# Performance work log

Measured on AMD Instinct MI355X. Metric: run time of the kernel, lower is better.

## Reference

```python
import jax, jax.numpy as jnp
import numpy as np

D = 128
RANK = 16
N_USER, N_PROD, N_CAT, N_BRAND = 100000, 100000, 1000, 2000
E_BEH, E_STR = 100000, 50000
NODE_TYPES = ['user', 'product', 'category', 'brand']
N_NODES = {'user': N_USER, 'product': N_PROD, 'category': N_CAT, 'brand': N_BRAND}
PHI = {'user': 0, 'product': 1, 'category': 2, 'brand': 3}
# (src_type, edge_name, dst_type, rel_idx, beta or None for structural)
EDGE_META = [
    ('user', 'view', 'product', 0, 0),
    ('user', 'cart', 'product', 1, 1),
    ('user', 'purchase', 'product', 2, 2),
    ('product', 'rev_view', 'user', 3, 0),
    ('product', 'rev_cart', 'user', 4, 1),
    ('product', 'rev_purchase', 'user', 5, 2),
    ('product', 'belongs_to', 'category', 6, None),
    ('category', 'contains', 'product', 7, None),
    ('product', 'producedBy', 'brand', 8, None),
    ('brand', 'brands', 'product', 9, None),
]


def setup_inputs() -> dict:
    key = jax.random.key(0)
    ks = iter(jax.random.split(key, 64))
    inp = {}
    for t in NODE_TYPES:
        inp['x_' + t] = jax.random.normal(next(ks), (N_NODES[t], D), jnp.float32)
    for (st, name, dt, ridx, beta) in EDGE_META:
        E = E_BEH if beta is not None else E_STR
        src = jax.random.randint(next(ks), (E,), 0, N_NODES[st], jnp.int32)
        dst = jax.random.randint(next(ks), (E,), 0, N_NODES[dt], jnp.int32)
        inp['ei_' + name] = jnp.stack([src, dst])
        if beta is None:
            inp['attr_' + name] = jax.random.randint(next(ks), (E,), 0, 3, jnp.int32)
    s = 0.05
    inp['W_base'] = jax.random.normal(next(ks), (D, D), jnp.float32) * s
    inp['A'] = jax.random.normal(next(ks), (4, D, RANK), jnp.float32) * s
    inp['B'] = jax.random.normal(next(ks), (4, D, RANK), jnp.float32) * s
    inp['rel_W'] = jax.random.normal(next(ks), (10, D), jnp.float32) * s
    inp['beh_W'] = jax.random.normal(next(ks), (4, D), jnp.float32) * s
    inp['a_att'] = jax.random.normal(next(ks), (4 * D,), jnp.float32) * s
    inp['ln_gamma'] = jnp.ones((D,), jnp.float32)
    inp['ln_beta'] = jnp.zeros((D,), jnp.float32)
    return inp


def _forward(x, eis, attrs, W_base, A, B, rel_W, beh_W, a_att, ln_gamma, ln_beta):
    a0, a1, a2, a3 = a_att[:D], a_att[D:2 * D], a_att[2 * D:3 * D], a_att[3 * D:]
    agg = {t: jnp.zeros((N_NODES[t], D), x['user'].dtype) for t in NODE_TYPES}
    for (src_t, name, dst_t, ridx, beta) in EDGE_META:
        ei = eis[name]
        src, dst = ei[0], ei[1]
        hs = x[src_t][src]            # [E, D] gather
        hd = x[dst_t][dst]            # [E, D] gather
        phi = PHI[src_t]
        if beta is not None:
            # uniform behavior beta: W = W_base + A_phi @ B_beta^T
            W = W_base + A[phi] @ B[beta].T
            msg = hs @ W.T
            hproj = hd @ W.T
            b_term = (beh_W[beta] * a3).sum()
        else:
            # per-edge behavior origin from edge_attr (clamped to {0,1,2})
            origin = jnp.clip(attrs[name].reshape(-1), 0, 2)
            mids = jnp.einsum('ei,bir->ebr', hs, B[:3])            # [E, 3, rank]
            mid = jnp.take_along_axis(mids, origin[:, None, None], axis=1)[:, 0, :]
            msg = hs @ W_base.T + mid @ A[phi].T
            hproj = hd @ W_base.T
            b_term = (beh_W[origin] * a3).sum(-1)                  # [E]
        r_scalar = (rel_W[ridx] * a2).sum()
        e = (msg * a0).sum(-1) + (hproj * a1).sum(-1) + r_scalar + b_term
        # destination-grouped softmax over edges
        n_dst = N_NODES[dst_t]
        m = jax.ops.segment_max(e, dst, num_segments=n_dst)
        ex = jnp.exp(e - m[dst])
        ssum = jax.ops.segment_sum(ex, dst, num_segments=n_dst)
        alpha = ex / (ssum[dst] + 1e-16)
        agg[dst_t] = agg[dst_t] + jax.ops.segment_sum(alpha[:, None] * msg, dst, num_segments=n_dst)
    outs = []
    for t in NODE_TYPES:
        h = agg[t]
        mu = h.mean(-1, keepdims=True)
        var = ((h - mu) ** 2).mean(-1, keepdims=True)
        hn = (h - mu) / jnp.sqrt(var + 1e-5) * ln_gamma + ln_beta
        outs.append(jax.nn.elu(hn + x[t]))   # residual: in_dim == out_dim
    return jnp.concatenate(outs, axis=0)     # [N_user+N_prod+N_cat+N_brand, D]


def reference(x_user, x_product, x_category, x_brand,
              ei_view, ei_cart, ei_purchase, ei_rev_view, ei_rev_cart, ei_rev_purchase,
              ei_belongs_to, ei_contains, ei_producedBy, ei_brands,
              attr_belongs_to, attr_contains, attr_producedBy, attr_brands,
              W_base, A, B, rel_W, beh_W, a_att, ln_gamma, ln_beta):
    x = {'user': x_user, 'product': x_product, 'category': x_category, 'brand': x_brand}
    eis = {'view': ei_view, 'cart': ei_cart, 'purchase': ei_purchase,
           'rev_view': ei_rev_view, 'rev_cart': ei_rev_cart, 'rev_purchase': ei_rev_purchase,
           'belongs_to': ei_belongs_to, 'contains': ei_contains,
           'producedBy': ei_producedBy, 'brands': ei_brands}
    attrs = {'belongs_to': attr_belongs_to, 'contains': attr_contains,
             'producedBy': attr_producedBy, 'brands': attr_brands}
    return _forward(x, eis, attrs, W_base, A, B, rel_W, beh_W, a_att, ln_gamma, ln_beta)
```

## Files before the change

kernel.cpp:

```cpp
#include <hip/hip_runtime.h>
#include <hip/hip_bf16.h>
#include <math.h>

#define D 128

#define NU 100000
#define NP 100000
#define NC 1000
#define NB 2000
#define NTOT 203000
#define EB 100000
#define ES 50000
#define ETOT 800000
#define NSEG 803000
#define NBLK 785

#define OFF_L    0
#define OFF_W0   6448000
#define OFF_BS   6451840
#define OFF_WT   7251856
#define OFF_AT   7268240
#define OFF_INT  7276432

__constant__ int c_srcT[10]   = {0,0,0,1,1,1,1,2,1,3};
__constant__ int c_phi [10]   = {0,0,0,1,1,1,1,2,1,3};
__constant__ int c_beta[10]   = {0,1,2,0,1,2,-1,-1,-1,-1};
__constant__ int c_E   [10]   = {EB,EB,EB,EB,EB,EB,ES,ES,ES,ES};
__constant__ int c_moff[10]   = {0,100000,200000,300000,400000,500000,600000,601000,701000,703000};

__constant__ int g_nGrp[4]    = {1,3,1,1};
__constant__ int g_Loff[4][3] = {{1600000,0,0},{0,3216000,4848000},{3200000,0,0},{4816000,0,0}};
__constant__ int g_ai[4][3]   = {{1,0,0},{0,2,3},{1,0,0},{1,0,0}};

#define K4_BU 782
#define K4_BP 1564
#define K4_BC 1572
#define K4_BT 1588

struct Ptrs {
    const float* x[4];
    const int*   ei[10];
    const int*   attr[4];
};

__device__ __forceinline__ void decode_et(int eflat, int& et, int& le) {
    if (eflat < 600000) { et = eflat / 100000; le = eflat - et * 100000; }
    else { int r = eflat - 600000; int q = r / 50000; et = 6 + q; le = r - q * 50000; }
}

__device__ __forceinline__ float qsum(float v) {
    v += __shfl_xor(v, 1, 64);
    v += __shfl_xor(v, 2, 64);
    v += __shfl_xor(v, 4, 64);
    v += __shfl_xor(v, 8, 64);
    return v;
}

__global__ void k0_tables(const float* __restrict__ Wb, const float* __restrict__ A,
                          const float* __restrict__ B, const float* __restrict__ behW,
                          const float* __restrict__ a_att,
                          float* __restrict__ w0, float* __restrict__ bs_out)
{
    __shared__ float a0[128];
    __shared__ float c0[128];
    __shared__ float g0[4][16];
    int t = threadIdx.x;
    if (t < 128) a0[t] = a_att[t];
    __syncthreads();
    if (t < 128) {
        float s0=0.f;
        for (int j=0;j<128;j++) s0 += Wb[j*128+t]*a0[j];
        c0[t]=s0;
    } else if (t < 192) {
        int q=t-128, p=q>>4, r=q&15;
        float s0=0.f;
        for (int i=0;i<128;i++) s0 += A[p*2048+i*16+r]*a0[i];
        g0[p][r]=s0;
    } else if (t < 196) {
        int b=t-192; float s=0.f;
        for (int i=0;i<128;i++) s += behW[b*128+i]*a_att[384+i];
        bs_out[b]=s;
    }
    __syncthreads();
    if (t < 128) {
        for (int et=0; et<10; ++et) {
            int phi=c_phi[et], beta=c_beta[et];
            if (beta >= 0) {
                float s0=c0[t];
                for (int r=0;r<16;r++) s0 += B[beta*2048+t*16+r]*g0[phi][r];
                w0[et*384+t]=s0; w0[et*384+128+t]=s0; w0[et*384+256+t]=s0;
            } else {
                for (int o=0;o<3;o++){
                    float s0=c0[t];
                    for (int r=0;r<16;r++) s0 += B[o*2048+t*16+r]*g0[phi][r];
                    w0[et*384+o*128+t]=s0;
                }
            }
        }
    }
}

__global__ __launch_bounds__(256) void ktrans(const float* __restrict__ Wb,
        const float* __restrict__ A, float* __restrict__ WbT, float* __restrict__ AT)
{
    int idx = blockIdx.x*256 + threadIdx.x;
    if (idx < 16384) { int i = idx>>7, j = idx&127; WbT[i*128+j] = Wb[j*128+i]; }
    int idx2 = idx - 16384;
    if (idx2 >= 0 && idx2 < 8192) {
        int p = idx2>>11, rem = idx2&2047, r = rem>>7, j = rem&127;
        AT[idx2] = A[p*2048 + j*16 + r];
    }
}

__global__ __launch_bounds__(256) void khist(Ptrs P, int* __restrict__ counts)
{
    int eflat = blockIdx.x*256 + threadIdx.x;
    if (eflat >= ETOT) return;
    int et, le; decode_et(eflat, et, le);
    int dst = P.ei[et][c_E[et] + le];
    atomicAdd(&counts[c_moff[et] + dst], 1);
}

__global__ __launch_bounds__(256) void kscan1(const int* __restrict__ cnt,
                                              int* __restrict__ st, int* __restrict__ bsums)
{
    __shared__ int lds[256];
    int t = threadIdx.x, b = blockIdx.x;
    int base = b*1024 + t*4;
    int v0 = (base   < NSEG) ? cnt[base]   : 0;
    int v1 = (base+1 < NSEG) ? cnt[base+1] : 0;
    int v2 = (base+2 < NSEG) ? cnt[base+2] : 0;
    int v3 = (base+3 < NSEG) ? cnt[base+3] : 0;
    int s = v0+v1+v2+v3;
    lds[t] = s; __syncthreads();
    for (int off=1; off<256; off<<=1){
        int xv = (t>=off) ? lds[t-off] : 0;
        __syncthreads();
        lds[t] += xv;
        __syncthreads();
    }
    int incl = lds[t];
    int p = incl - s;
    if (t==255) bsums[b] = incl;
    if (base   < NSEG) st[base]   = p; p += v0;
    if (base+1 < NSEG) st[base+1] = p; p += v1;
    if (base+2 < NSEG) st[base+2] = p; p += v2;
    if (base+3 < NSEG) st[base+3] = p;
}

__global__ __launch_bounds__(256) void kscan2(int* __restrict__ bsums)
{
    __shared__ int lds[256];
    int t = threadIdx.x;
    int base = t*4;
    int v0 = (base   < NBLK) ? bsums[base]   : 0;
    int v1 = (base+1 < NBLK) ? bsums[base+1] : 0;
    int v2 = (base+2 < NBLK) ? bsums[base+2] : 0;
    int v3 = (base+3 < NBLK) ? bsums[base+3] : 0;
    int s = v0+v1+v2+v3;
    lds[t] = s; __syncthreads();
    for (int off=1; off<256; off<<=1){
        int xv = (t>=off) ? lds[t-off] : 0;
        __syncthreads();
        lds[t] += xv;
        __syncthreads();
    }
    int p = lds[t] - s;
    if (base   < NBLK) bsums[base]   = p; p += v0;
    if (base+1 < NBLK) bsums[base+1] = p; p += v1;
    if (base+2 < NBLK) bsums[base+2] = p; p += v2;
    if (base+3 < NBLK) bsums[base+3] = p;
}

__global__ __launch_bounds__(256) void kscan3(int* __restrict__ st, const int* __restrict__ bsums)
{
    int t = threadIdx.x, b = blockIdx.x;
    int add = bsums[b];
    int base = b*1024 + t*4;
    #pragma unroll
    for (int j=0;j<4;j++)
        if (base+j < NSEG) st[base+j] += add;
}

__global__ __launch_bounds__(256) void kscatter(Ptrs P, int* __restrict__ st, int* __restrict__ srco)
{
    int eflat = blockIdx.x*256 + threadIdx.x;
    if (eflat >= ETOT) return;
    int et, le; decode_et(eflat, et, le);
    const int* ei = P.ei[et];
    int E = c_E[et];
    int src = ei[le], dst = ei[E+le];
    int o;
    if (et >= 6) { int a = P.attr[et-6][le]; o = min(max(a,0),2); }
    else o = c_beta[et];
    int pos = atomicAdd(&st[c_moff[et] + dst], 1);
    srco[pos] = src | (o<<17) | (et<<19);
}

__global__ __launch_bounds__(256) void kagg_beh(Ptrs P,
        const int* __restrict__ starts, const int* __restrict__ counts,
        const int* __restrict__ srco,
        const float* __restrict__ w0, const float* __restrict__ Bm,
        float* __restrict__ Sout, float* __restrict__ Lb, int nWaves)
{
    int lane = threadIdx.x & 63;
    int wv = (blockIdx.x * 256 + threadIdx.x) >> 6;
    int grp = lane >> 4, ln = lane & 15;

    for (int nid = wv; nid < NU + NP; nid += nWaves) {
        int T = (nid < NU) ? 0 : 1;
        int n0 = (T == 0) ? nid : nid - NU;
        int etBase = (T == 0) ? 3 : 0;
        const float* xs = P.x[1 - T];

        int sgA = c_moff[etBase] + n0;
        int cnt0 = counts[sgA],        cnt1 = counts[sgA+100000], cnt2 = counts[sgA+200000];
        int sa0  = starts[sgA]-cnt0,   sa1  = starts[sgA+100000]-cnt1, sa2 = starts[sgA+200000]-cnt2;
        int sv1 = (grp < cnt1) ? srco[sa1+grp] : 0;
        int sv2 = (grp < cnt2) ? srco[sa2+grp] : 0;
        float4 pA = make_float4(0.f,0.f,0.f,0.f), pB = pA;
        if (grp < cnt0) {
            int sv0 = srco[sa0+grp];
            const float* q = xs + (size_t)(sv0 & 0x1FFFF)*D + ln*8;
            pA = *(const float4*)q; pB = *(const float4*)(q+4);
        }

        float Stot[8] = {0,0,0,0,0,0,0,0};
        float Lq0=0.f, Lq1=0.f, Lq2=0.f, Lq3=0.f;

        for (int s=0; s<3; ++s) {
            int cnt = (s==0)?cnt0:((s==1)?cnt1:cnt2);
            int st0 = (s==0)?sa0:((s==1)?sa1:sa2);
            float4 cA = pA, cB = pB;
            pA = make_float4(0.f,0.f,0.f,0.f); pB = pA;
            if (s == 0) {
                if (grp < cnt1) {
                    const float* q = xs + (size_t)(sv1 & 0x1FFFF)*D + ln*8;
                    pA = *(const float4*)q; pB = *(const float4*)(q+4);
                }
            } else if (s == 1) {
                if (grp < cnt2) {
                    const float* q = xs + (size_t)(sv2 & 0x1FFFF)*D + ln*8;
                    pA = *(const float4*)q; pB = *(const float4*)(q+4);
                }
            }
            if (cnt == 0) continue;
            int et = etBase + s;
            const float* wq = w0 + et*384 + ln*8;
            float4 wA = *(const float4*)wq, wB = *(const float4*)(wq+4);

            float ssum = 0.f;
            float SA[8] = {0,0,0,0,0,0,0,0};

            for (int k0=0; k0<cnt; k0+=4) {
                bool act = (k0+grp) < cnt;
                if (k0 > 0) {
                    cA = make_float4(0.f,0.f,0.f,0.f); cB = cA;
                    if (act) {
                        int sv = srco[st0+k0+grp];
                        const float* q = xs + (size_t)(sv & 0x1FFFF)*D + ln*8;
                        cA = *(const float4*)q; cB = *(const float4*)(q+4);
                    }
                }
                float d = cA.x*wA.x + cA.y*wA.y + cA.z*wA.z + cA.w*wA.w
                        + cB.x*wB.x + cB.y*wB.y + cB.z*wB.z + cB.w*wB.w;
                d = qsum(d);
                float wg = act ? __expf(d) : 0.f;
                ssum += wg;
                SA[0]+=wg*cA.x; SA[1]+=wg*cA.y; SA[2]+=wg*cA.z; SA[3]+=wg*cA.w;
                SA[4]+=wg*cB.x; SA[5]+=wg*cB.y; SA[6]+=wg*cB.z; SA[7]+=wg*cB.w;
            }
            ssum += __shfl_xor(ssum, 16, 64);
            ssum += __shfl_xor(ssum, 32, 64);
            float inv = 1.f/(ssum + 1e-16f);
            #pragma unroll
            for (int j=0;j<8;j++){ SA[j] += __shfl_xor(SA[j],16,64); SA[j] += __shfl_xor(SA[j],32,64); }
            #pragma unroll
            for (int j=0;j<8;j++) Stot[j] += SA[j]*inv;

            const float* Bp = Bm + s*2048 + grp*4;
            float p0=0.f,p1=0.f,p2=0.f,p3=0.f;
            #pragma unroll
            for (int j=0;j<8;j++){
                float4 b4 = *(const float4*)(Bp + (ln*8+j)*16);
                float v = SA[j];
                p0+=v*b4.x; p1+=v*b4.y; p2+=v*b4.z; p3+=v*b4.w;
            }
            Lq0 += qsum(p0)*inv; Lq1 += qsum(p1)*inv;
            Lq2 += qsum(p2)*inv; Lq3 += qsum(p3)*inv;
        }

        if (grp == 0) {
            float* Srow = Sout + (size_t)nid*D + ln*8;
            *(float4*)Srow     = make_float4(Stot[0],Stot[1],Stot[2],Stot[3]);
            *(float4*)(Srow+4) = make_float4(Stot[4],Stot[5],Stot[6],Stot[7]);
        }
        if (ln < 4) {
            float v = (ln==0)?Lq0:((ln==1)?Lq1:((ln==2)?Lq2:Lq3));
            int loff = (T==0) ? 1600000 : 0;
            Lb[loff + (size_t)n0*16 + grp*4 + ln] = v;
        }
    }
}

__global__ __launch_bounds__(256) void kagg_str(Ptrs P,
        const int* __restrict__ starts, const int* __restrict__ counts,
        const int* __restrict__ srco,
        const float* __restrict__ w0, const float* __restrict__ bs,
        const float* __restrict__ Bm,
        float* __restrict__ Sout, float* __restrict__ Lb, int nWaves)
{
    int lane = threadIdx.x & 63;
    int wv = (blockIdx.x * 256 + threadIdx.x) >> 6;
    int grp = lane >> 4, ln = lane & 15;
    float bs0 = bs[0], bs1 = bs[1], bs2 = bs[2];

    for (int id = wv; id < NP + NC + NB; id += nWaves) {
        int T, n0, nseg;
        if (id < NP) { T=1; n0=id; nseg=2; }
        else if (id < NP+NC) { T=2; n0=id-NP; nseg=1; }
        else { T=3; n0=id-(NP+NC); nseg=1; }
        int outRow = (T==1) ? (100000+n0) : ((T==2) ? (200000+n0) : (201000+n0));

        float Stot[8] = {0,0,0,0,0,0,0,0};

        for (int s=0; s<nseg; ++s) {
            int et = (T==1) ? (s==0 ? 7 : 9) : ((T==2) ? 6 : 8);
            int seg = c_moff[et] + n0;
            int cnt = counts[seg];
            int st0 = starts[seg] - cnt;
            const float* xs = P.x[c_srcT[et]];
            const float* wbase = w0 + et*384;

            float ssum = 0.f;
            float SA[8]={0,0,0,0,0,0,0,0}, SB[8]={0,0,0,0,0,0,0,0}, SC[8]={0,0,0,0,0,0,0,0};
            int fa=0, fb=0, fc=0;

            for (int k0=0; k0<cnt; k0+=4) {
                bool act = (k0+grp) < cnt;
                int sv = act ? srco[st0+k0+grp] : 0;
                int o = (sv>>17)&3;
                float4 hA = make_float4(0.f,0.f,0.f,0.f), hB = hA;
                if (act) {
                    const float* q = xs + (size_t)(sv & 0x1FFFF)*D + ln*8;
                    hA = *(const float4*)q; hB = *(const float4*)(q+4);
                }
                const float* wq = wbase + o*128 + ln*8;
                float4 wA = *(const float4*)wq, wB = *(const float4*)(wq+4);
                float d = hA.x*wA.x + hA.y*wA.y + hA.z*wA.z + hA.w*wA.w
                        + hB.x*wB.x + hB.y*wB.y + hB.z*wB.z + hB.w*wB.w;
                d = qsum(d);
                float wg = act ? __expf(d + ((o==0)?bs0:((o==1)?bs1:bs2))) : 0.f;
                ssum += wg;
                fa |= (int)(act && (o==0)); fb |= (int)(act && (o==1)); fc |= (int)(act && (o==2));
                float wg0=(o==0)?wg:0.f, wg1=(o==1)?wg:0.f, wg2=(o==2)?wg:0.f;
                #pragma unroll
                for (int j=0;j<8;j++){
                    float hj = (j==0)?hA.x:(j==1)?hA.y:(j==2)?hA.z:(j==3)?hA.w:
                               (j==4)?hB.x:(j==5)?hB.y:(j==6)?hB.z:hB.w;
                    SA[j] += wg0*hj; SB[j] += wg1*hj; SC[j] += wg2*hj;
                }
            }

            ssum += __shfl_xor(ssum, 16, 64);
            ssum += __shfl_xor(ssum, 32, 64);
            float inv = 1.f/(ssum + 1e-16f);

            int anyA = __any(fa), anyB = __any(fb), anyC = __any(fc);
            if (anyA) {
                #pragma unroll
                for (int j=0;j<8;j++){ SA[j] += __shfl_xor(SA[j],16,64); SA[j] += __shfl_xor(SA[j],32,64); }
            }
            if (anyB) {
                #pragma unroll
                for (int j=0;j<8;j++){ SB[j] += __shfl_xor(SB[j],16,64); SB[j] += __shfl_xor(SB[j],32,64); }
            }
            if (anyC) {
                #pragma unroll
                for (int j=0;j<8;j++){ SC[j] += __shfl_xor(SC[j],16,64); SC[j] += __shfl_xor(SC[j],32,64); }
            }
            #pragma unroll
            for (int j=0;j<8;j++) Stot[j] += (SA[j]+SB[j]+SC[j])*inv;

            float p0=0.f,p1=0.f,p2=0.f,p3=0.f;
            if (anyA) {
                const float* Bp = Bm + grp*4;
                #pragma unroll
                for (int j=0;j<8;j++){
                    float4 b4 = *(const float4*)(Bp + (ln*8+j)*16);
                    float v = SA[j];
                    p0+=v*b4.x; p1+=v*b4.y; p2+=v*b4.z; p3+=v*b4.w;
                }
            }
            if (anyB) {
                const float* Bp = Bm + 2048 + grp*4;
                #pragma unroll
                for (int j=0;j<8;j++){
                    float4 b4 = *(const float4*)(Bp + (ln*8+j)*16);
                    float v = SB[j];
                    p0+=v*b4.x; p1+=v*b4.y; p2+=v*b4.z; p3+=v*b4.w;
                }
            }
            if (anyC) {
                const float* Bp = Bm + 4096 + grp*4;
                #pragma unroll
                for (int j=0;j<8;j++){
                    float4 b4 = *(const float4*)(Bp + (ln*8+j)*16);
                    float v = SC[j];
                    p0+=v*b4.x; p1+=v*b4.y; p2+=v*b4.z; p3+=v*b4.w;
                }
            }
            p0 = qsum(p0)*inv; p1 = qsum(p1)*inv; p2 = qsum(p2)*inv; p3 = qsum(p3)*inv;

            int loff = (T==1) ? (s==0 ? 3216000 : 4848000) : ((T==2) ? 3200000 : 4816000);
            if (ln < 4) {
                float v = (ln==0)?p0:((ln==1)?p1:((ln==2)?p2:p3));
                Lb[loff + (size_t)n0*16 + grp*4 + ln] = v;
            }
        }

        if (grp == 0) {
            float* Srow = Sout + (size_t)outRow*D + ln*8;
            if (T == 1) {
                float4 a = *(const float4*)Srow, b = *(const float4*)(Srow+4);
                *(float4*)Srow     = make_float4(a.x+Stot[0],a.y+Stot[1],a.z+Stot[2],a.w+Stot[3]);
                *(float4*)(Srow+4) = make_float4(b.x+Stot[4],b.y+Stot[5],b.z+Stot[6],b.w+Stot[7]);
            } else {
                *(float4*)Srow     = make_float4(Stot[0],Stot[1],Stot[2],Stot[3]);
                *(float4*)(Srow+4) = make_float4(Stot[4],Stot[5],Stot[6],Stot[7]);
            }
        }
    }
}

__global__ __launch_bounds__(512, 1) void k4_final(Ptrs P,
        const float* __restrict__ WbT, const float* __restrict__ AT,
        const float* __restrict__ Lb,
        const float* __restrict__ gamma, const float* __restrict__ lbeta,
        float* __restrict__ out)
{
    __shared__ float st[128*132];
    __shared__ float wt[128*128];
    __shared__ float lt[128*52];
    int t = threadIdx.x;
    int b = blockIdx.x;
    int T, lb;
    if (b < K4_BU)      { T=0; lb=b; }
    else if (b < K4_BP) { T=1; lb=b-K4_BU; }
    else if (b < K4_BC) { T=2; lb=b-K4_BP; }
    else                { T=3; lb=b-K4_BC; }
    int r0 = lb*128;
    int rowStart = (T==0)?0:((T==1)?100000:((T==2)?200000:201000));
    int nRows    = (T==0)?NU:((T==1)?NP:((T==2)?NC:NB));
    const float* x = P.x[T];
    int nPairs = g_nGrp[T];

    for (int idx=t; idx<4096; idx+=512)
        *(float4*)&wt[idx*4] = *(const float4*)&WbT[idx*4];
    for (int idx=t; idx<4096; idx+=512){
        int r = idx>>5, i4 = idx&31;
        int lr = r0 + r;
        float4 v = (lr < nRows) ? *(const float4*)&out[(size_t)(rowStart+lr)*D + i4*4]
                                : make_float4(0.f,0.f,0.f,0.f);
        *(float4*)&st[r*132 + i4*4] = v;
    }
    for (int pi=0; pi<nPairs; ++pi){
        int lo = g_Loff[T][pi];
        int r = t>>2, q = t&3;
        int lr = r0 + r;
        float4 v = (lr < nRows) ? *(const float4*)&Lb[lo + (size_t)lr*16 + q*4]
                                : make_float4(0.f,0.f,0.f,0.f);
        *(float4*)&lt[r*52 + pi*16 + q*4] = v;
    }
    __syncthreads();

    int cg = t & 15, rg = t >> 4;
    float acc[4][8];
    #pragma unroll
    for (int a=0;a<4;a++)
        #pragma unroll
        for (int c=0;c<8;c++) acc[a][c]=0.f;

    for (int i4=0; i4<32; ++i4){
        float4 sv0 = *(const float4*)&st[(rg*4+0)*132 + i4*4];
        float4 sv1 = *(const float4*)&st[(rg*4+1)*132 + i4*4];
        float4 sv2 = *(const float4*)&st[(rg*4+2)*132 + i4*4];
        float4 sv3 = *(const float4*)&st[(rg*4+3)*132 + i4*4];
        #pragma unroll
        for (int q=0;q<4;q++){
            float4 wA = *(const float4*)&wt[(i4*4+q)*128 + cg*4];
            float4 wB = *(const float4*)&wt[(i4*4+q)*128 + 64 + cg*4];
            float sq[4];
            sq[0] = (q==0)?sv0.x:(q==1)?sv0.y:(q==2)?sv0.z:sv0.w;
            sq[1] = (q==0)?sv1.x:(q==1)?sv1.y:(q==2)?sv1.z:sv1.w;
            sq[2] = (q==0)?sv2.x:(q==1)?sv2.y:(q==2)?sv2.z:sv2.w;
            sq[3] = (q==0)?sv3.x:(q==1)?sv3.y:(q==2)?sv3.z:sv3.w;
            #pragma unroll
            for (int rr=0;rr<4;rr++){
                acc[rr][0] += sq[rr]*wA.x;
                acc[rr][1] += sq[rr]*wA.y;
                acc[rr][2] += sq[rr]*wA.z;
                acc[rr][3] += sq[rr]*wA.w;
                acc[rr][4] += sq[rr]*wB.x;
                acc[rr][5] += sq[rr]*wB.y;
                acc[rr][6] += sq[rr]*wB.z;
                acc[rr][7] += sq[rr]*wB.w;
            }
        }
    }

    for (int pi=0; pi<nPairs; ++pi){
        int ai = g_ai[T][pi];
        const float* Ap = AT + ai*2048;
        #pragma unroll 4
        for (int r=0;r<16;++r){
            float4 aA = *(const float4*)&Ap[r*128 + cg*4];
            float4 aB = *(const float4*)&Ap[r*128 + 64 + cg*4];
            float lv[4];
            #pragma unroll
            for (int rr=0;rr<4;rr++) lv[rr] = lt[(rg*4+rr)*52 + pi*16 + r];
            #pragma unroll
            for (int rr=0;rr<4;rr++){
                acc[rr][0] += lv[rr]*aA.x;
                acc[rr][1] += lv[rr]*aA.y;
                acc[rr][2] += lv[rr]*aA.z;
                acc[rr][3] += lv[rr]*aA.w;
                acc[rr][4] += lv[rr]*aB.x;
                acc[rr][5] += lv[rr]*aB.y;
                acc[rr][6] += lv[rr]*aB.z;
                acc[rr][7] += lv[rr]*aB.w;
            }
        }
    }

    int jA = cg*4, jB = 64 + cg*4;
    float4 gA = *(const float4*)&gamma[jA], gB = *(const float4*)&gamma[jB];
    float4 bA = *(const float4*)&lbeta[jA], bB = *(const float4*)&lbeta[jB];
    float gv[8] = {gA.x,gA.y,gA.z,gA.w,gB.x,gB.y,gB.z,gB.w};
    float bv[8] = {bA.x,bA.y,bA.z,bA.w,bB.x,bB.y,bB.z,bB.w};

    #pragma unroll
    for (int rr=0;rr<4;rr++){
        int lr = r0 + rg*4 + rr;
        float lsum=0.f, lsq=0.f;
        #pragma unroll
        for (int c=0;c<8;c++){ lsum += acc[rr][c]; lsq += acc[rr][c]*acc[rr][c]; }
        #pragma unroll
        for (int mm=1; mm<16; mm<<=1){ lsum += __shfl_xor(lsum,mm,64); lsq += __shfl_xor(lsq,mm,64); }
        if (lr >= nRows) continue;
        float mu = lsum*(1.f/128.f);
        float var = lsq*(1.f/128.f) - mu*mu;
        float rstd = rsqrtf(var + 1e-5f);
        const float* xr = x + (size_t)lr*D;
        float4 xA = *(const float4*)(xr+jA), xB = *(const float4*)(xr+jB);
        float xv[8] = {xA.x,xA.y,xA.z,xA.w,xB.x,xB.y,xB.z,xB.w};
        float ov[8];
        #pragma unroll
        for (int c=0;c<8;c++){
            float hn = (acc[rr][c]-mu)*rstd*gv[c] + bv[c];
            float z = hn + xv[c];
            ov[c] = z > 0.f ? z : expm1f(z);
        }
        float* orow = out + (size_t)(rowStart+lr)*D;
        *(float4*)(orow+jA) = make_float4(ov[0],ov[1],ov[2],ov[3]);
        *(float4*)(orow+jB) = make_float4(ov[4],ov[5],ov[6],ov[7]);
    }
}

extern "C" void kernel_launch(void* const* d_in, const int* in_sizes, int n_in,
                              void* d_out, int out_size, void* d_ws, size_t ws_size,
                              hipStream_t stream)
{
    (void)in_sizes; (void)n_in; (void)out_size; (void)ws_size;
    Ptrs P;
    P.x[0] = (const float*)d_in[0];
    P.x[1] = (const float*)d_in[1];
    P.x[2] = (const float*)d_in[2];
    P.x[3] = (const float*)d_in[3];
    P.ei[0] = (const int*)d_in[4];
    P.ei[1] = (const int*)d_in[5];
    P.ei[2] = (const int*)d_in[6];
    P.ei[3] = (const int*)d_in[7];
    P.ei[4] = (const int*)d_in[8];
    P.ei[5] = (const int*)d_in[9];
    P.ei[6] = (const int*)d_in[10];
    P.attr[0] = (const int*)d_in[11];
    P.ei[7] = (const int*)d_in[12];
    P.attr[1] = (const int*)d_in[13];
    P.ei[8] = (const int*)d_in[14];
    P.attr[2] = (const int*)d_in[15];
    P.ei[9] = (const int*)d_in[16];
    P.attr[3] = (const int*)d_in[17];
    const float* Wb    = (const float*)d_in[18];
    const float* A     = (const float*)d_in[19];
    const float* B     = (const float*)d_in[20];
    const float* behW  = (const float*)d_in[22];
    const float* a_att = (const float*)d_in[23];
    const float* gamma = (const float*)d_in[24];
    const float* lbeta = (const float*)d_in[25];
    float* wsf = (float*)d_ws;
    float* out = (float*)d_out;

    int* ip     = (int*)(wsf + OFF_INT);
    int* counts = ip;
    int* starts = ip + 803000;
    int* srco   = ip + 1606000;
    int* bsums  = (int*)wsf;

    hipMemsetAsync(counts, 0, (size_t)NSEG*sizeof(int), stream);

    k0_tables<<<1, 256, 0, stream>>>(Wb, A, B, behW, a_att, wsf+OFF_W0, wsf+OFF_BS);
    ktrans<<<96, 256, 0, stream>>>(Wb, A, wsf+OFF_WT, wsf+OFF_AT);
    khist<<<3125, 256, 0, stream>>>(P, counts);
    kscan1<<<NBLK, 256, 0, stream>>>(counts, starts, bsums);
    kscan2<<<1, 256, 0, stream>>>(bsums);
    kscan3<<<NBLK, 256, 0, stream>>>(starts, bsums);
    kscatter<<<3125, 256, 0, stream>>>(P, starts, srco);

    kagg_beh<<<2048, 256, 0, stream>>>(P, starts, counts, srco,
                                       wsf+OFF_W0, B, out, wsf+OFF_L, 2048*4);
    kagg_str<<<1024, 256, 0, stream>>>(P, starts, counts, srco,
                                       wsf+OFF_W0, wsf+OFF_BS, B, out, wsf+OFF_L, 1024*4);

    k4_final<<<K4_BT, 512, 0, stream>>>(P, wsf+OFF_WT, wsf+OFF_AT, wsf+OFF_L,
                                        gamma, lbeta, out);
}
```

Measured before the change: 893.3 us.

## Use atomic work-stealing tickets and batched metadata prefetch in behavior aggregation

Replaces the static grid-stride node loop in the behavior aggregation kernel with dynamic scheduling. Each wavefront grabs a ticket for a chunk of four nodes through an atomic counter. All counts and starts for the chunk are loaded cooperatively in one step and shared by shuffles, and the first source indices of the next node are prefetched while the current node is processed. The aim is to balance the irregular per-node degree load and hide metadata latency, at the cost of one global atomic per chunk and an extra memset.

Result: slower. 1.169 ms (+30.9%).

```diff
diff --git a/kernel.cpp b/kernel.cpp
--- a/kernel.cpp
+++ b/kernel.cpp
@@ -201,104 +201,147 @@
         const int* __restrict__ starts, const int* __restrict__ counts,
         const int* __restrict__ srco,
         const float* __restrict__ w0, const float* __restrict__ Bm,
-        float* __restrict__ Sout, float* __restrict__ Lb, int nWaves)
+        float* __restrict__ Sout, float* __restrict__ Lb, int* __restrict__ ticket)
 {
     int lane = threadIdx.x & 63;
-    int wv = (blockIdx.x * 256 + threadIdx.x) >> 6;
     int grp = lane >> 4, ln = lane & 15;
 
-    for (int nid = wv; nid < NU + NP; nid += nWaves) {
-        int T = (nid < NU) ? 0 : 1;
-        int n0 = (T == 0) ? nid : nid - NU;
-        int etBase = (T == 0) ? 3 : 0;
-        const float* xs = P.x[1 - T];
-
-        int sgA = c_moff[etBase] + n0;
-        int cnt0 = counts[sgA],        cnt1 = counts[sgA+100000], cnt2 = counts[sgA+200000];
-        int sa0  = starts[sgA]-cnt0,   sa1  = starts[sgA+100000]-cnt1, sa2 = starts[sgA+200000]-cnt2;
-        int sv1 = (grp < cnt1) ? srco[sa1+grp] : 0;
-        int sv2 = (grp < cnt2) ? srco[sa2+grp] : 0;
-        float4 pA = make_float4(0.f,0.f,0.f,0.f), pB = pA;
-        if (grp < cnt0) {
-            int sv0 = srco[sa0+grp];
-            const float* q = xs + (size_t)(sv0 & 0x1FFFF)*D + ln*8;
-            pA = *(const float4*)q; pB = *(const float4*)(q+4);
-        }
-
-        float Stot[8] = {0,0,0,0,0,0,0,0};
-        float Lq0=0.f, Lq1=0.f, Lq2=0.f, Lq3=0.f;
-
-        for (int s=0; s<3; ++s) {
-            int cnt = (s==0)?cnt0:((s==1)?cnt1:cnt2);
-            int st0 = (s==0)?sa0:((s==1)?sa1:sa2);
-            float4 cA = pA, cB = pB;
-            pA = make_float4(0.f,0.f,0.f,0.f); pB = pA;
-            if (s == 0) {
-                if (grp < cnt1) {
-                    const float* q = xs + (size_t)(sv1 & 0x1FFFF)*D + ln*8;
-                    pA = *(const float4*)q; pB = *(const float4*)(q+4);
-                }
-            } else if (s == 1) {
-                if (grp < cnt2) {
-                    const float* q = xs + (size_t)(sv2 & 0x1FFFF)*D + ln*8;
-                    pA = *(const float4*)q; pB = *(const float4*)(q+4);
-                }
-            }
-            if (cnt == 0) continue;
-            int et = etBase + s;
-            const float* wq = w0 + et*384 + ln*8;
-            float4 wA = *(const float4*)wq, wB = *(const float4*)(wq+4);
-
-            float ssum = 0.f;
-            float SA[8] = {0,0,0,0,0,0,0,0};
-
-            for (int k0=0; k0<cnt; k0+=4) {
-                bool act = (k0+grp) < cnt;
-                if (k0 > 0) {
-                    cA = make_float4(0.f,0.f,0.f,0.f); cB = cA;
-                    if (act) {
-                        int sv = srco[st0+k0+grp];
-                        const float* q = xs + (size_t)(sv & 0x1FFFF)*D + ln*8;
-                        cA = *(const float4*)q; cB = *(const float4*)(q+4);
+    for (;;) {
+        int chunk = 0;
+        if (lane == 0) chunk = atomicAdd(ticket, 1);
+        chunk = __shfl(chunk, 0, 64);
+        int base = chunk << 2;
+        if (base >= NU + NP) return;
+
+        int si = 0;
+        {
+            int j = lane / 6, r = lane - j*6;
+            if (lane < 24) {
+                int nid = base + j;
+                if (nid < NU + NP) {
+                    int s = r >> 1;
+                    int seg = ((nid < NU) ? (300000 + nid) : (nid - NU)) + s*100000;
+                    si = (r & 1) ? starts[seg] : counts[seg];
+                }
+            }
+        }
+
+        int sv0 = 0, sv1 = 0, sv2 = 0;
+        {
+            int c0 = __shfl(si, 0, 64), t0 = __shfl(si, 1, 64);
+            int c1 = __shfl(si, 2, 64), t1 = __shfl(si, 3, 64);
+            int c2 = __shfl(si, 4, 64), t2 = __shfl(si, 5, 64);
+            if (grp < c0) sv0 = srco[t0 - c0 + grp];
+            if (grp < c1) sv1 = srco[t1 - c1 + grp];
+            if (grp < c2) sv2 = srco[t2 - c2 + grp];
+        }
+
+        for (int j = 0; j < 4; ++j) {
+            int nid = base + j;
+            if (nid >= NU + NP) break;
+            int T = (nid < NU) ? 0 : 1;
+            int n0 = (T == 0) ? nid : nid - NU;
+            int etBase = (T == 0) ? 3 : 0;
+            const float* xs = P.x[1 - T];
+
+            int c0 = __shfl(si, j*6+0, 64), t0 = __shfl(si, j*6+1, 64);
+            int c1 = __shfl(si, j*6+2, 64), t1 = __shfl(si, j*6+3, 64);
+            int c2 = __shfl(si, j*6+4, 64), t2 = __shfl(si, j*6+5, 64);
+            int sa0 = t0 - c0, sa1 = t1 - c1, sa2 = t2 - c2;
+
+            int nv0 = 0, nv1 = 0, nv2 = 0;
+            if (j < 3 && base + j + 1 < NU + NP) {
+                int d0 = __shfl(si, j*6+6,  64), u0 = __shfl(si, j*6+7,  64);
+                int d1 = __shfl(si, j*6+8,  64), u1 = __shfl(si, j*6+9,  64);
+                int d2 = __shfl(si, j*6+10, 64), u2 = __shfl(si, j*6+11, 64);
+                if (grp < d0) nv0 = srco[u0 - d0 + grp];
+                if (grp < d1) nv1 = srco[u1 - d1 + grp];
+                if (grp < d2) nv2 = srco[u2 - d2 + grp];
+            }
+
+            float4 pA = make_float4(0.f,0.f,0.f,0.f), pB = pA;
+            if (grp < c0) {
+                const float* q = xs + (size_t)(sv0 & 0x1FFFF)*D + ln*8;
+                pA = *(const float4*)q; pB = *(const float4*)(q+4);
+            }
+
+            float Stot[8] = {0,0,0,0,0,0,0,0};
+            float Lq0=0.f, Lq1=0.f, Lq2=0.f, Lq3=0.f;
+
+            for (int s = 0; s < 3; ++s) {
+                int cnt = (s==0)?c0:((s==1)?c1:c2);
+                int st0 = (s==0)?sa0:((s==1)?sa1:sa2);
+                float4 cA = pA, cB = pB;
+                pA = make_float4(0.f,0.f,0.f,0.f); pB = pA;
+                if (s == 0) {
+                    if (grp < c1) {
+                        const float* q = xs + (size_t)(sv1 & 0x1FFFF)*D + ln*8;
+                        pA = *(const float4*)q; pB = *(const float4*)(q+4);
                     }
-                }
-                float d = cA.x*wA.x + cA.y*wA.y + cA.z*wA.z + cA.w*wA.w
-                        + cB.x*wB.x + cB.y*wB.y + cB.z*wB.z + cB.w*wB.w;
-                d = qsum(d);
-                float wg = act ? __expf(d) : 0.f;
-                ssum += wg;
-                SA[0]+=wg*cA.x; SA[1]+=wg*cA.y; SA[2]+=wg*cA.z; SA[3]+=wg*cA.w;
-                SA[4]+=wg*cB.x; SA[5]+=wg*cB.y; SA[6]+=wg*cB.z; SA[7]+=wg*cB.w;
-            }
-            ssum += __shfl_xor(ssum, 16, 64);
-            ssum += __shfl_xor(ssum, 32, 64);
-            float inv = 1.f/(ssum + 1e-16f);
-            #pragma unroll
-            for (int j=0;j<8;j++){ SA[j] += __shfl_xor(SA[j],16,64); SA[j] += __shfl_xor(SA[j],32,64); }
-            #pragma unroll
-            for (int j=0;j<8;j++) Stot[j] += SA[j]*inv;
-
-            const float* Bp = Bm + s*2048 + grp*4;
-            float p0=0.f,p1=0.f,p2=0.f,p3=0.f;
-            #pragma unroll
-            for (int j=0;j<8;j++){
-                float4 b4 = *(const float4*)(Bp + (ln*8+j)*16);
-                float v = SA[j];
-                p0+=v*b4.x; p1+=v*b4.y; p2+=v*b4.z; p3+=v*b4.w;
-            }
-            Lq0 += qsum(p0)*inv; Lq1 += qsum(p1)*inv;
-            Lq2 += qsum(p2)*inv; Lq3 += qsum(p3)*inv;
-        }
-
-        if (grp == 0) {
-            float* Srow = Sout + (size_t)nid*D + ln*8;
-            *(float4*)Srow     = make_float4(Stot[0],Stot[1],Stot[2],Stot[3]);
-            *(float4*)(Srow+4) = make_float4(Stot[4],Stot[5],Stot[6],Stot[7]);
-        }
-        if (ln < 4) {
-            float v = (ln==0)?Lq0:((ln==1)?Lq1:((ln==2)?Lq2:Lq3));
-            int loff = (T==0) ? 1600000 : 0;
-            Lb[loff + (size_t)n0*16 + grp*4 + ln] = v;
+                } else if (s == 1) {
+                    if (grp < c2) {
+                        const float* q = xs + (size_t)(sv2 & 0x1FFFF)*D + ln*8;
+                        pA = *(const float4*)q; pB = *(const float4*)(q+4);
+                    }
+                }
+                if (cnt == 0) continue;
+                int et = etBase + s;
+                const float* wq = w0 + et*384 + ln*8;
+                float4 wA = *(const float4*)wq, wB = *(const float4*)(wq+4);
+
+                float ssum = 0.f;
+                float SA[8] = {0,0,0,0,0,0,0,0};
+
+                for (int k0 = 0; k0 < cnt; k0 += 4) {
+                    bool act = (k0 + grp) < cnt;
+                    if (k0 > 0) {
+                        cA = make_float4(0.f,0.f,0.f,0.f); cB = cA;
+                        if (act) {
+                            int sv = srco[st0 + k0 + grp];
+                            const float* q = xs + (size_t)(sv & 0x1FFFF)*D + ln*8;
+                            cA = *(const float4*)q; cB = *(const float4*)(q+4);
+                        }
+                    }
+                    float d = cA.x*wA.x + cA.y*wA.y + cA.z*wA.z + cA.w*wA.w
+                            + cB.x*wB.x + cB.y*wB.y + cB.z*wB.z + cB.w*wB.w;
+                    d = qsum(d);
+                    float wg = act ? __expf(d) : 0.f;
+                    ssum += wg;
+                    SA[0]+=wg*cA.x; SA[1]+=wg*cA.y; SA[2]+=wg*cA.z; SA[3]+=wg*cA.w;
+                    SA[4]+=wg*cB.x; SA[5]+=wg*cB.y; SA[6]+=wg*cB.z; SA[7]+=wg*cB.w;
+                }
+                ssum += __shfl_xor(ssum, 16, 64);
+                ssum += __shfl_xor(ssum, 32, 64);
+                float inv = 1.f/(ssum + 1e-16f);
+                #pragma unroll
+                for (int jj=0;jj<8;jj++){ SA[jj] += __shfl_xor(SA[jj],16,64); SA[jj] += __shfl_xor(SA[jj],32,64); }
+                #pragma unroll
+                for (int jj=0;jj<8;jj++) Stot[jj] += SA[jj]*inv;
+
+                const float* Bp = Bm + s*2048 + grp*4;
+                float p0=0.f,p1=0.f,p2=0.f,p3=0.f;
+                #pragma unroll
+                for (int jj=0;jj<8;jj++){
+                    float4 b4 = *(const float4*)(Bp + (ln*8+jj)*16);
+                    float v = SA[jj];
+                    p0+=v*b4.x; p1+=v*b4.y; p2+=v*b4.z; p3+=v*b4.w;
+                }
+                Lq0 += qsum(p0)*inv; Lq1 += qsum(p1)*inv;
+                Lq2 += qsum(p2)*inv; Lq3 += qsum(p3)*inv;
+            }
+
+            if (grp == 0) {
+                float* Srow = Sout + (size_t)nid*D + ln*8;
+                *(float4*)Srow     = make_float4(Stot[0],Stot[1],Stot[2],Stot[3]);
+                *(float4*)(Srow+4) = make_float4(Stot[4],Stot[5],Stot[6],Stot[7]);
+            }
+            if (ln < 4) {
+                float v = (ln==0)?Lq0:((ln==1)?Lq1:((ln==2)?Lq2:Lq3));
+                int loff = (T==0) ? 1600000 : 0;
+                Lb[loff + (size_t)n0*16 + grp*4 + ln] = v;
+            }
+
+            sv0 = nv0; sv1 = nv1; sv2 = nv2;
         }
     }
 }
@@ -605,9 +648,11 @@
     int* counts = ip;
     int* starts = ip + 803000;
     int* srco   = ip + 1606000;
+    int* ticket = ip + 2406000;
     int* bsums  = (int*)wsf;
 
     hipMemsetAsync(counts, 0, (size_t)NSEG*sizeof(int), stream);
+    hipMemsetAsync(ticket, 0, sizeof(int), stream);
 
     k0_tables<<<1, 256, 0, stream>>>(Wb, A, B, behW, a_att, wsf+OFF_W0, wsf+OFF_BS);
     ktrans<<<96, 256, 0, stream>>>(Wb, A, wsf+OFF_WT, wsf+OFF_AT);
@@ -618,7 +663,7 @@
     kscatter<<<3125, 256, 0, stream>>>(P, starts, srco);
 
     kagg_beh<<<2048, 256, 0, stream>>>(P, starts, counts, srco,
-                                       wsf+OFF_W0, B, out, wsf+OFF_L, 2048*4);
+                                       wsf+OFF_W0, B, out, wsf+OFF_L, ticket);
     kagg_str<<<1024, 256, 0, stream>>>(P, starts, counts, srco,
                                        wsf+OFF_W0, wsf+OFF_BS, B, out, wsf+OFF_L, 1024*4);
 
```

## Map one node per 16-lane group in behavioral aggregation with per-edge prefetch

Applied to the files above, without the earlier changes.

The behavioral aggregation kernel now gives each wave four nodes, one per 16-lane group, instead of one node spread over four groups. Each group walks its edges one at a time and prefetches the next source row. This removes the cross-group shuffle reductions and idle lanes when a node has few edges. Segment metadata is loaded cooperatively and broadcast with shuffles. The low-rank B projection becomes a transpose-style shuffle reduction so each lane ends up with one output. The cost is serial per-edge latency inside each group and divergence when the four nodes have very different degrees.

Result: slower. 1.070 ms (+19.7%).

```diff
diff --git a/kernel.cpp b/kernel.cpp
--- a/kernel.cpp
+++ b/kernel.cpp
@@ -54,6 +54,39 @@
     v += __shfl_xor(v, 4, 64);
     v += __shfl_xor(v, 8, 64);
     return v;
+}
+
+__device__ __forceinline__ float bT_pass8(const float* __restrict__ Brow,
+                                          const float SA[8], int c0, int lane)
+{
+    float pr[8] = {0.f,0.f,0.f,0.f,0.f,0.f,0.f,0.f};
+    #pragma unroll
+    for (int j=0;j<8;j++){
+        float4 b0 = *(const float4*)(Brow + j*16 + c0);
+        float4 b1 = *(const float4*)(Brow + j*16 + c0 + 4);
+        float v = SA[j];
+        pr[0]+=v*b0.x; pr[1]+=v*b0.y; pr[2]+=v*b0.z; pr[3]+=v*b0.w;
+        pr[4]+=v*b1.x; pr[5]+=v*b1.y; pr[6]+=v*b1.z; pr[7]+=v*b1.w;
+    }
+    #pragma unroll
+    for (int r=0;r<8;r++) pr[r] += __shfl_xor(pr[r], 8, 64);
+    float v4[4];
+    #pragma unroll
+    for (int r=0;r<4;r++){
+        float kp = (lane&4) ? pr[r+4] : pr[r];
+        float gv = (lane&4) ? pr[r]   : pr[r+4];
+        v4[r] = kp + __shfl_xor(gv, 4, 64);
+    }
+    float v2[2];
+    #pragma unroll
+    for (int r=0;r<2;r++){
+        float kp = (lane&2) ? v4[r+2] : v4[r];
+        float gv = (lane&2) ? v4[r]   : v4[r+2];
+        v2[r] = kp + __shfl_xor(gv, 2, 64);
+    }
+    float kp = (lane&1) ? v2[1] : v2[0];
+    float gv = (lane&1) ? v2[0] : v2[1];
+    return kp + __shfl_xor(gv, 1, 64);
 }
 
 __global__ void k0_tables(const float* __restrict__ Wb, const float* __restrict__ A,
@@ -204,47 +237,56 @@
         float* __restrict__ Sout, float* __restrict__ Lb, int nWaves)
 {
     int lane = threadIdx.x & 63;
-    int wv = (blockIdx.x * 256 + threadIdx.x) >> 6;
+    int wv = (blockIdx.x*256 + threadIdx.x) >> 6;
     int grp = lane >> 4, ln = lane & 15;
-
-    for (int nid = wv; nid < NU + NP; nid += nWaves) {
-        int T = (nid < NU) ? 0 : 1;
-        int n0 = (T == 0) ? nid : nid - NU;
-        int etBase = (T == 0) ? 3 : 0;
+    int slotBase = grp << 4;
+
+    const int NTOTB = NU + NP;
+    const int nGroups = (NTOTB + 3) >> 2;
+
+    for (int g = wv; g < nGroups; g += nWaves) {
+        int nid = g*4 + grp;
+        bool have = nid < NTOTB;
+        int T = (have && nid >= NU) ? 1 : 0;
+        int n0 = (T==0) ? nid : nid - NU;
+        int etBase = (T==0) ? 3 : 0;
         const float* xs = P.x[1 - T];
 
-        int sgA = c_moff[etBase] + n0;
-        int cnt0 = counts[sgA],        cnt1 = counts[sgA+100000], cnt2 = counts[sgA+200000];
-        int sa0  = starts[sgA]-cnt0,   sa1  = starts[sgA+100000]-cnt1, sa2 = starts[sgA+200000]-cnt2;
-        int sv1 = (grp < cnt1) ? srco[sa1+grp] : 0;
-        int sv2 = (grp < cnt2) ? srco[sa2+grp] : 0;
+        int c_l = 0, e_l = 0, h_l = 0;
+        if (have && ln < 3) {
+            int seg = c_moff[etBase] + n0 + ln*100000;
+            c_l = counts[seg];
+            e_l = starts[seg];
+            if (c_l > 0) h_l = srco[e_l - c_l];
+        }
+        int cnt0 = __shfl(c_l, slotBase+0, 64), cnt1 = __shfl(c_l, slotBase+1, 64), cnt2 = __shfl(c_l, slotBase+2, 64);
+        int end0 = __shfl(e_l, slotBase+0, 64), end1 = __shfl(e_l, slotBase+1, 64), end2 = __shfl(e_l, slotBase+2, 64);
+        int sv0  = __shfl(h_l, slotBase+0, 64), sv1  = __shfl(h_l, slotBase+1, 64), sv2  = __shfl(h_l, slotBase+2, 64);
+        int sa0 = end0-cnt0, sa1 = end1-cnt1, sa2 = end2-cnt2;
+
         float4 pA = make_float4(0.f,0.f,0.f,0.f), pB = pA;
-        if (grp < cnt0) {
-            int sv0 = srco[sa0+grp];
+        if (cnt0 > 0) {
             const float* q = xs + (size_t)(sv0 & 0x1FFFF)*D + ln*8;
             pA = *(const float4*)q; pB = *(const float4*)(q+4);
         }
 
         float Stot[8] = {0,0,0,0,0,0,0,0};
-        float Lq0=0.f, Lq1=0.f, Lq2=0.f, Lq3=0.f;
-
+        float Lacc = 0.f;
+
+        #pragma unroll
         for (int s=0; s<3; ++s) {
             int cnt = (s==0)?cnt0:((s==1)?cnt1:cnt2);
             int st0 = (s==0)?sa0:((s==1)?sa1:sa2);
             float4 cA = pA, cB = pB;
             pA = make_float4(0.f,0.f,0.f,0.f); pB = pA;
-            if (s == 0) {
-                if (grp < cnt1) {
-                    const float* q = xs + (size_t)(sv1 & 0x1FFFF)*D + ln*8;
-                    pA = *(const float4*)q; pB = *(const float4*)(q+4);
-                }
-            } else if (s == 1) {
-                if (grp < cnt2) {
-                    const float* q = xs + (size_t)(sv2 & 0x1FFFF)*D + ln*8;
-                    pA = *(const float4*)q; pB = *(const float4*)(q+4);
-                }
-            }
-            if (cnt == 0) continue;
+            if (s == 0 && cnt1 > 0) {
+                const float* q = xs + (size_t)(sv1 & 0x1FFFF)*D + ln*8;
+                pA = *(const float4*)q; pB = *(const float4*)(q+4);
+            } else if (s == 1 && cnt2 > 0) {
+                const float* q = xs + (size_t)(sv2 & 0x1FFFF)*D + ln*8;
+                pA = *(const float4*)q; pB = *(const float4*)(q+4);
+            }
+
             int et = etBase + s;
             const float* wq = w0 + et*384 + ln*8;
             float4 wA = *(const float4*)wq, wB = *(const float4*)(wq+4);
@@ -252,53 +294,41 @@
             float ssum = 0.f;
             float SA[8] = {0,0,0,0,0,0,0,0};
 
-            for (int k0=0; k0<cnt; k0+=4) {
-                bool act = (k0+grp) < cnt;
-                if (k0 > 0) {
-                    cA = make_float4(0.f,0.f,0.f,0.f); cB = cA;
-                    if (act) {
-                        int sv = srco[st0+k0+grp];
-                        const float* q = xs + (size_t)(sv & 0x1FFFF)*D + ln*8;
-                        cA = *(const float4*)q; cB = *(const float4*)(q+4);
-                    }
+            for (int k=0; k<cnt; ++k) {
+                float4 nA = make_float4(0.f,0.f,0.f,0.f), nB = nA;
+                if (k+1 < cnt) {
+                    int svn = srco[st0+k+1];
+                    const float* q = xs + (size_t)(svn & 0x1FFFF)*D + ln*8;
+                    nA = *(const float4*)q; nB = *(const float4*)(q+4);
                 }
                 float d = cA.x*wA.x + cA.y*wA.y + cA.z*wA.z + cA.w*wA.w
                         + cB.x*wB.x + cB.y*wB.y + cB.z*wB.z + cB.w*wB.w;
                 d = qsum(d);
-                float wg = act ? __expf(d) : 0.f;
+                float wg = __expf(d);
                 ssum += wg;
                 SA[0]+=wg*cA.x; SA[1]+=wg*cA.y; SA[2]+=wg*cA.z; SA[3]+=wg*cA.w;
                 SA[4]+=wg*cB.x; SA[5]+=wg*cB.y; SA[6]+=wg*cB.z; SA[7]+=wg*cB.w;
-            }
-            ssum += __shfl_xor(ssum, 16, 64);
-            ssum += __shfl_xor(ssum, 32, 64);
+                cA = nA; cB = nB;
+            }
             float inv = 1.f/(ssum + 1e-16f);
             #pragma unroll
-            for (int j=0;j<8;j++){ SA[j] += __shfl_xor(SA[j],16,64); SA[j] += __shfl_xor(SA[j],32,64); }
-            #pragma unroll
             for (int j=0;j<8;j++) Stot[j] += SA[j]*inv;
 
-            const float* Bp = Bm + s*2048 + grp*4;
-            float p0=0.f,p1=0.f,p2=0.f,p3=0.f;
-            #pragma unroll
-            for (int j=0;j<8;j++){
-                float4 b4 = *(const float4*)(Bp + (ln*8+j)*16);
-                float v = SA[j];
-                p0+=v*b4.x; p1+=v*b4.y; p2+=v*b4.z; p3+=v*b4.w;
-            }
-            Lq0 += qsum(p0)*inv; Lq1 += qsum(p1)*inv;
-            Lq2 += qsum(p2)*inv; Lq3 += qsum(p3)*inv;
-        }
-
-        if (grp == 0) {
+            if (__any(cnt > 0)) {
+                const float* Brow = Bm + s*2048 + (ln*8)*16;
+                float r1 = bT_pass8(Brow, SA, 0, lane);
+                float r2 = bT_pass8(Brow, SA, 8, lane);
+                float Lv = (ln & 8) ? r2 : r1;
+                Lacc += Lv * inv;
+            }
+        }
+
+        if (have) {
             float* Srow = Sout + (size_t)nid*D + ln*8;
             *(float4*)Srow     = make_float4(Stot[0],Stot[1],Stot[2],Stot[3]);
             *(float4*)(Srow+4) = make_float4(Stot[4],Stot[5],Stot[6],Stot[7]);
-        }
-        if (ln < 4) {
-            float v = (ln==0)?Lq0:((ln==1)?Lq1:((ln==2)?Lq2:Lq3));
             int loff = (T==0) ? 1600000 : 0;
-            Lb[loff + (size_t)n0*16 + grp*4 + ln] = v;
+            Lb[loff + (size_t)n0*16 + ln] = Lacc;
         }
     }
 }
```

## Skip empty product segments, prefetch edge loads, and widen behavior aggregation grid

Applied to the files above, without the earlier changes.

Splits the structural aggregation into a product path and a category/brand path. The product path returns early when both incoming segments are empty, which relies on a new memset that zeroes the L buffer so skipped nodes read as zero. It also preloads the first source index per segment. The category/brand path software-pipelines the next group of gathered rows, and the behavior kernel launches with twice as many blocks. The cost is an extra memset of about 26 MB and higher register pressure.

Measured after the change: 872.8 us. 1.02x faster.

```diff
diff --git a/kernel.cpp b/kernel.cpp
--- a/kernel.cpp
+++ b/kernel.cpp
@@ -303,6 +303,98 @@
     }
 }
 
+__device__ __forceinline__ void str_seg_prod(int cnt, int st0, int hv,
+        const int* __restrict__ srco, const float* __restrict__ xs,
+        const float* __restrict__ wbase, float bs0, float bs1, float bs2,
+        const float* __restrict__ Bm, int grp, int ln,
+        float Stot[8], float* __restrict__ Lrow)
+{
+    if (cnt == 0) return;
+    float ssum = 0.f;
+    float SA[8]={0,0,0,0,0,0,0,0}, SB[8]={0,0,0,0,0,0,0,0}, SC[8]={0,0,0,0,0,0,0,0};
+    int fa=0, fb=0, fc=0;
+
+    for (int k0=0; k0<cnt; k0+=4) {
+        bool act = (k0+grp) < cnt;
+        int sv = (k0 == 0) ? hv : (act ? srco[st0+k0+grp] : 0);
+        int o = (sv>>17)&3;
+        float4 hA = make_float4(0.f,0.f,0.f,0.f), hB = hA;
+        if (act) {
+            const float* q = xs + (size_t)(sv & 0x1FFFF)*D + ln*8;
+            hA = *(const float4*)q; hB = *(const float4*)(q+4);
+        }
+        const float* wq = wbase + o*128 + ln*8;
+        float4 wA = *(const float4*)wq, wB = *(const float4*)(wq+4);
+        float d = hA.x*wA.x + hA.y*wA.y + hA.z*wA.z + hA.w*wA.w
+                + hB.x*wB.x + hB.y*wB.y + hB.z*wB.z + hB.w*wB.w;
+        d = qsum(d);
+        float wg = act ? __expf(d + ((o==0)?bs0:((o==1)?bs1:bs2))) : 0.f;
+        ssum += wg;
+        fa |= (int)(act && (o==0)); fb |= (int)(act && (o==1)); fc |= (int)(act && (o==2));
+        float wg0=(o==0)?wg:0.f, wg1=(o==1)?wg:0.f, wg2=(o==2)?wg:0.f;
+        #pragma unroll
+        for (int j=0;j<8;j++){
+            float hj = (j==0)?hA.x:(j==1)?hA.y:(j==2)?hA.z:(j==3)?hA.w:
+                       (j==4)?hB.x:(j==5)?hB.y:(j==6)?hB.z:hB.w;
+            SA[j] += wg0*hj; SB[j] += wg1*hj; SC[j] += wg2*hj;
+        }
+    }
+
+    ssum += __shfl_xor(ssum, 16, 64);
+    ssum += __shfl_xor(ssum, 32, 64);
+    float inv = 1.f/(ssum + 1e-16f);
+
+    int anyA = __any(fa), anyB = __any(fb), anyC = __any(fc);
+    if (anyA) {
+        #pragma unroll
+        for (int j=0;j<8;j++){ SA[j] += __shfl_xor(SA[j],16,64); SA[j] += __shfl_xor(SA[j],32,64); }
+    }
+    if (anyB) {
+        #pragma unroll
+        for (int j=0;j<8;j++){ SB[j] += __shfl_xor(SB[j],16,64); SB[j] += __shfl_xor(SB[j],32,64); }
+    }
+    if (anyC) {
+        #pragma unroll
+        for (int j=0;j<8;j++){ SC[j] += __shfl_xor(SC[j],16,64); SC[j] += __shfl_xor(SC[j],32,64); }
+    }
+    #pragma unroll
+    for (int j=0;j<8;j++) Stot[j] += (SA[j]+SB[j]+SC[j])*inv;
+
+    float p0=0.f,p1=0.f,p2=0.f,p3=0.f;
+    if (anyA) {
+        const float* Bp = Bm + grp*4;
+        #pragma unroll
+        for (int j=0;j<8;j++){
+            float4 b4 = *(const float4*)(Bp + (ln*8+j)*16);
+            float v = SA[j];
+            p0+=v*b4.x; p1+=v*b4.y; p2+=v*b4.z; p3+=v*b4.w;
+        }
+    }
+    if (anyB) {
+        const float* Bp = Bm + 2048 + grp*4;
+        #pragma unroll
+        for (int j=0;j<8;j++){
+            float4 b4 = *(const float4*)(Bp + (ln*8+j)*16);
+            float v = SB[j];
+            p0+=v*b4.x; p1+=v*b4.y; p2+=v*b4.z; p3+=v*b4.w;
+        }
+    }
+    if (anyC) {
+        const float* Bp = Bm + 4096 + grp*4;
+        #pragma unroll
+        for (int j=0;j<8;j++){
+            float4 b4 = *(const float4*)(Bp + (ln*8+j)*16);
+            float v = SC[j];
+            p0+=v*b4.x; p1+=v*b4.y; p2+=v*b4.z; p3+=v*b4.w;
+        }
+    }
+    p0 = qsum(p0)*inv; p1 = qsum(p1)*inv; p2 = qsum(p2)*inv; p3 = qsum(p3)*inv;
+    if (ln < 4) {
+        float v = (ln==0)?p0:((ln==1)?p1:((ln==2)?p2:p3));
+        Lrow[grp*4 + ln] = v;
+    }
+}
+
 __global__ __launch_bounds__(256) void kagg_str(Ptrs P,
         const int* __restrict__ starts, const int* __restrict__ counts,
         const int* __restrict__ srco,
@@ -316,35 +408,61 @@
     float bs0 = bs[0], bs1 = bs[1], bs2 = bs[2];
 
     for (int id = wv; id < NP + NC + NB; id += nWaves) {
-        int T, n0, nseg;
-        if (id < NP) { T=1; n0=id; nseg=2; }
-        else if (id < NP+NC) { T=2; n0=id-NP; nseg=1; }
-        else { T=3; n0=id-(NP+NC); nseg=1; }
-        int outRow = (T==1) ? (100000+n0) : ((T==2) ? (200000+n0) : (201000+n0));
-
-        float Stot[8] = {0,0,0,0,0,0,0,0};
-
-        for (int s=0; s<nseg; ++s) {
-            int et = (T==1) ? (s==0 ? 7 : 9) : ((T==2) ? 6 : 8);
+        if (id < NP) {
+            int n0 = id;
+            int seg7 = 601000 + n0, seg9 = 703000 + n0;
+            int cnt7 = counts[seg7], cnt9 = counts[seg9];
+            if ((cnt7 | cnt9) == 0) continue;
+            int st7 = starts[seg7] - cnt7, st9 = starts[seg9] - cnt9;
+            int hv7 = (grp < cnt7) ? srco[st7+grp] : 0;
+            int hv9 = (grp < cnt9) ? srco[st9+grp] : 0;
+
+            float Stot[8] = {0,0,0,0,0,0,0,0};
+            str_seg_prod(cnt7, st7, hv7, srco, P.x[2], w0 + 7*384,
+                         bs0, bs1, bs2, Bm, grp, ln, Stot,
+                         Lb + 3216000 + (size_t)n0*16);
+            str_seg_prod(cnt9, st9, hv9, srco, P.x[3], w0 + 9*384,
+                         bs0, bs1, bs2, Bm, grp, ln, Stot,
+                         Lb + 4848000 + (size_t)n0*16);
+
+            if (grp == 0) {
+                float* Srow = Sout + (size_t)(100000+n0)*D + ln*8;
+                float4 a = *(const float4*)Srow, b = *(const float4*)(Srow+4);
+                *(float4*)Srow     = make_float4(a.x+Stot[0],a.y+Stot[1],a.z+Stot[2],a.w+Stot[3]);
+                *(float4*)(Srow+4) = make_float4(b.x+Stot[4],b.y+Stot[5],b.z+Stot[6],b.w+Stot[7]);
+            }
+        } else {
+            int T = (id < NP+NC) ? 2 : 3;
+            int n0 = (T==2) ? (id-NP) : (id-(NP+NC));
+            int et = (T==2) ? 6 : 8;
+            int outRow = (T==2) ? (200000+n0) : (201000+n0);
             int seg = c_moff[et] + n0;
             int cnt = counts[seg];
             int st0 = starts[seg] - cnt;
-            const float* xs = P.x[c_srcT[et]];
+            const float* xs = P.x[1];
             const float* wbase = w0 + et*384;
 
             float ssum = 0.f;
             float SA[8]={0,0,0,0,0,0,0,0}, SB[8]={0,0,0,0,0,0,0,0}, SC[8]={0,0,0,0,0,0,0,0};
             int fa=0, fb=0, fc=0;
 
+            int sv = 0;
+            float4 hA = make_float4(0.f,0.f,0.f,0.f), hB = hA;
+            if (grp < cnt) {
+                sv = srco[st0+grp];
+                const float* q = xs + (size_t)(sv & 0x1FFFF)*D + ln*8;
+                hA = *(const float4*)q; hB = *(const float4*)(q+4);
+            }
             for (int k0=0; k0<cnt; k0+=4) {
+                int svn = 0;
+                float4 nA = make_float4(0.f,0.f,0.f,0.f), nB = nA;
+                if (k0+4+grp < cnt) {
+                    svn = srco[st0+k0+4+grp];
+                    const float* q = xs + (size_t)(svn & 0x1FFFF)*D + ln*8;
+                    nA = *(const float4*)q; nB = *(const float4*)(q+4);
+                }
                 bool act = (k0+grp) < cnt;
-                int sv = act ? srco[st0+k0+grp] : 0;
                 int o = (sv>>17)&3;
-                float4 hA = make_float4(0.f,0.f,0.f,0.f), hB = hA;
-                if (act) {
-                    const float* q = xs + (size_t)(sv & 0x1FFFF)*D + ln*8;
-                    hA = *(const float4*)q; hB = *(const float4*)(q+4);
-                }
                 const float* wq = wbase + o*128 + ln*8;
                 float4 wA = *(const float4*)wq, wB = *(const float4*)(wq+4);
                 float d = hA.x*wA.x + hA.y*wA.y + hA.z*wA.z + hA.w*wA.w
@@ -360,6 +478,7 @@
                                (j==4)?hB.x:(j==5)?hB.y:(j==6)?hB.z:hB.w;
                     SA[j] += wg0*hj; SB[j] += wg1*hj; SC[j] += wg2*hj;
                 }
+                sv = svn; hA = nA; hB = nB;
             }
 
             ssum += __shfl_xor(ssum, 16, 64);
@@ -379,8 +498,9 @@
                 #pragma unroll
                 for (int j=0;j<8;j++){ SC[j] += __shfl_xor(SC[j],16,64); SC[j] += __shfl_xor(SC[j],32,64); }
             }
+            float Stot[8];
             #pragma unroll
-            for (int j=0;j<8;j++) Stot[j] += (SA[j]+SB[j]+SC[j])*inv;
+            for (int j=0;j<8;j++) Stot[j] = (SA[j]+SB[j]+SC[j])*inv;
 
             float p0=0.f,p1=0.f,p2=0.f,p3=0.f;
             if (anyA) {
@@ -412,20 +532,13 @@
             }
             p0 = qsum(p0)*inv; p1 = qsum(p1)*inv; p2 = qsum(p2)*inv; p3 = qsum(p3)*inv;
 
-            int loff = (T==1) ? (s==0 ? 3216000 : 4848000) : ((T==2) ? 3200000 : 4816000);
+            int loff = (T==2) ? 3200000 : 4816000;
             if (ln < 4) {
                 float v = (ln==0)?p0:((ln==1)?p1:((ln==2)?p2:p3));
                 Lb[loff + (size_t)n0*16 + grp*4 + ln] = v;
             }
-        }
-
-        if (grp == 0) {
-            float* Srow = Sout + (size_t)outRow*D + ln*8;
-            if (T == 1) {
-                float4 a = *(const float4*)Srow, b = *(const float4*)(Srow+4);
-                *(float4*)Srow     = make_float4(a.x+Stot[0],a.y+Stot[1],a.z+Stot[2],a.w+Stot[3]);
-                *(float4*)(Srow+4) = make_float4(b.x+Stot[4],b.y+Stot[5],b.z+Stot[6],b.w+Stot[7]);
-            } else {
+            if (grp == 0) {
+                float* Srow = Sout + (size_t)outRow*D + ln*8;
                 *(float4*)Srow     = make_float4(Stot[0],Stot[1],Stot[2],Stot[3]);
                 *(float4*)(Srow+4) = make_float4(Stot[4],Stot[5],Stot[6],Stot[7]);
             }
@@ -608,6 +721,7 @@
     int* bsums  = (int*)wsf;
 
     hipMemsetAsync(counts, 0, (size_t)NSEG*sizeof(int), stream);
+    hipMemsetAsync(wsf + OFF_L, 0, (size_t)6448000*sizeof(float), stream);
 
     k0_tables<<<1, 256, 0, stream>>>(Wb, A, B, behW, a_att, wsf+OFF_W0, wsf+OFF_BS);
     ktrans<<<96, 256, 0, stream>>>(Wb, A, wsf+OFF_WT, wsf+OFF_AT);
@@ -617,8 +731,8 @@
     kscan3<<<NBLK, 256, 0, stream>>>(starts, bsums);
     kscatter<<<3125, 256, 0, stream>>>(P, starts, srco);
 
-    kagg_beh<<<2048, 256, 0, stream>>>(P, starts, counts, srco,
-                                       wsf+OFF_W0, B, out, wsf+OFF_L, 2048*4);
+    kagg_beh<<<4096, 256, 0, stream>>>(P, starts, counts, srco,
+                                       wsf+OFF_W0, B, out, wsf+OFF_L, 4096*4);
     kagg_str<<<1024, 256, 0, stream>>>(P, starts, counts, srco,
                                        wsf+OFF_W0, wsf+OFF_BS, B, out, wsf+OFF_L, 1024*4);
 
```
